# Optimization experiments

Measured on AMD Instinct MI355X. Metric: run time of the kernel, lower is better.

The kernel has to match this reference:

```python
import jax, jax.numpy as jnp
import numpy as np
from jax import lax

G, N, S, K, R = 8, 4096, 2048, 64, 0.4   # graphs, nodes/graph, fps samples (ratio=0.5), max neighbors, radius
EPER = 65536                              # edges per graph (avg degree 16)
C = 13                                    # num_classes


def setup_inputs():
    key = jax.random.key(0)
    ks = jax.random.split(key, 8)
    norm = jax.random.normal(ks[0], (G * N, 3), jnp.float32)
    pos = jax.random.uniform(ks[1], (G * N, 3), jnp.float32)
    x = jax.random.normal(ks[2], (G * N, 2), jnp.float32)
    e = jax.random.randint(ks[3], (2, G, EPER), 0, N)
    off = (jnp.arange(G) * N)[None, :, None]
    edge_index = (e + off).reshape(2, G * EPER).astype(jnp.int64)
    batch = jnp.repeat(jnp.arange(G), N).astype(jnp.int64)
    def lin(k, i, o):
        return jax.random.normal(k, (i, o), jnp.float32) / np.float32(np.sqrt(i))
    W1 = lin(ks[4], 8, 64);    b1 = jnp.zeros((64,), jnp.float32)
    W2 = lin(ks[5], 72, 128);  b2 = jnp.zeros((128,), jnp.float32)
    W3 = lin(ks[6], 139, 256); b3 = jnp.zeros((256,), jnp.float32)
    lin_w = lin(ks[7], 256, C); lin_b = jnp.zeros((C,), jnp.float32)
    return dict(norm=norm, pos=pos, x=x, edge_index=edge_index, batch=batch,
                W1=W1, b1=b1, W2=W2, b2=b2, W3=W3, b3=b3, lin_w=lin_w, lin_b=lin_b)


def _gcn(h, src, dst, ew, W, b, n):
    # GCNConv(normalize=False): out[dst] += ew * (h @ W)[src]; + bias
    m = (h @ W)[src] * ew[:, None]
    return jax.ops.segment_sum(m, dst, num_segments=n) + b


def _fps(p):  # farthest point sampling on one graph, p: [N,3] -> [S] local indices (start at node 0)
    def step(carry, _):
        mind, cur = carry
        d = jnp.sum((p - p[cur]) ** 2, axis=1)
        mind = jnp.minimum(mind, d)
        return (mind, jnp.argmax(mind).astype(jnp.int32)), cur
    _, idx = lax.scan(step, (jnp.full((N,), jnp.inf, p.dtype), jnp.int32(0)), None, length=S)
    return idx


def _radius(p, q):  # p [N,3], q [S,3] -> neighbor cols [S,K] (lowest-index-first within radius), valid mask
    d2 = jnp.sum((q[:, None, :] - p[None, :, :]) ** 2, axis=-1)  # [S,N]
    mask = d2 < R * R
    score = jnp.where(mask, N - jnp.arange(N, dtype=jnp.int32)[None, :], 0)
    vals, cols = lax.top_k(score, K)
    valid = vals > 0
    return jnp.where(valid, cols, 0), valid


def reference(norm, pos, x, edge_index, batch, W1, b1, W2, b2, W3, b3, lin_w, lin_b):
    NT = G * N
    inp = jnp.concatenate([norm, pos, x], axis=1)          # [NT, 8]
    src, dst = edge_index[0], edge_index[1]
    ew = jnp.ones((src.shape[0],), inp.dtype)
    # dropout is inactive at inference (training=False)
    h1 = jax.nn.relu(_gcn(inp, src, dst, ew, W1, b1, NT))  # [NT, 64]
    h1 = jnp.concatenate([h1, inp], axis=1)                # [NT, 72]
    h2 = jax.nn.relu(_gcn(h1, src, dst, ew, W2, b2, NT))   # [NT, 128]

    pg = pos.reshape(G, N, 3)
    pgs = lax.stop_gradient(pg)
    idx_loc = jax.vmap(_fps)(pgs)                          # [G, S] local indices
    q = jax.vmap(lambda p, i: p[i])(pg, idx_loc)           # [G, S, 3] sampled positions
    cols, valid = jax.vmap(_radius)(pgs, lax.stop_gradient(q))  # [G, S, K]

    # PointConv with identity local_nn/global_nn: max over neighbors of [x_j, pos_j - pos_i]
    hg = h2.reshape(G, N, 128)
    def pconv(h, p, qv, c, v):
        msg = jnp.concatenate([h[c], p[c] - qv[:, None, :]], axis=-1)  # [S, K, 131]
        msg = jnp.where(v[..., None], msg, -jnp.inf)
        return jnp.max(msg, axis=1)                                    # [S, 131]
    x_int = jax.vmap(pconv)(hg, pg, q, cols, valid).reshape(G * S, 131)

    # filter_adj: keep edges with both endpoints sampled, remap to new ids
    idx_flat = (idx_loc + (jnp.arange(G) * N)[:, None]).reshape(-1)    # [G*S] global indices
    mapping = jnp.full((NT,), -1, jnp.int32).at[idx_flat].set(jnp.arange(G * S, dtype=jnp.int32))
    ns, nd = mapping[src], mapping[dst]
    em = (ns >= 0) & (nd >= 0)
    ew3 = em.astype(inp.dtype)
    ns = jnp.where(em, ns, 0)
    nd = jnp.where(em, nd, 0)

    h3in = jnp.concatenate([x_int, inp[idx_flat]], axis=1)  # [G*S, 139]
    h3 = jax.nn.relu(_gcn(h3in, ns, nd, ew3, W3, b3, G * S))  # [G*S, 256]

    pooled = h3.reshape(G, S, 256).max(axis=1)              # global_max_pool -> [G, 256]
    logits = pooled @ lin_w + lin_b
    out = jax.nn.log_softmax(logits, axis=1)
    pred = jax.nn.softmax(out, axis=1)
    return (out, pred)
```

## Files before the change

### kernel.cpp

```cpp
#include <hip/hip_runtime.h>
#include <hip/hip_bf16.h>

constexpr int NG   = 8;
constexpr int NPG  = 4096;
constexpr int NT   = NG * NPG;
constexpr int NS   = 2048;
constexpr int GS   = NG * NS;
constexpr int KN   = 64;
constexpr int NE   = NG * 65536;
constexpr int NC   = 13;

__device__ __forceinline__ float inp_val(const float* norm, const float* pos, const float* x,
                                         int node, int dim) {
  if (dim < 3) return norm[(size_t)node * 3 + dim];
  if (dim < 6) return pos[(size_t)node * 3 + (dim - 3)];
  return x[(size_t)node * 2 + (dim - 6)];
}

__global__ void feat1_kernel(const float* __restrict__ norm, const float* __restrict__ pos,
                             const float* __restrict__ x, const float* __restrict__ W1,
                             float* __restrict__ t1) {
  int n = blockIdx.x, f = threadIdx.x;
  __shared__ float row[8];
  if (f < 8) row[f] = inp_val(norm, pos, x, n, f);
  __syncthreads();
  float acc = 0.f;
#pragma unroll
  for (int i = 0; i < 8; ++i) acc += row[i] * W1[i * 64 + f];
  t1[(size_t)n * 64 + f] = acc;
}

__global__ void feat2_kernel(const float* __restrict__ h1, const float* __restrict__ norm,
                             const float* __restrict__ pos, const float* __restrict__ x,
                             const float* __restrict__ W2, float* __restrict__ t2) {
  int n = blockIdx.x, f = threadIdx.x;
  __shared__ float row[72];
  if (f < 64) row[f] = h1[(size_t)n * 64 + f];
  else if (f < 72) row[f] = inp_val(norm, pos, x, n, f - 64);
  __syncthreads();
  float acc = 0.f;
#pragma unroll 8
  for (int i = 0; i < 72; ++i) acc += row[i] * W2[i * 128 + f];
  t2[(size_t)n * 128 + f] = acc;
}

__global__ void feat3_kernel(const float* __restrict__ xint, const int* __restrict__ idxf,
                             const float* __restrict__ norm, const float* __restrict__ pos,
                             const float* __restrict__ x, const float* __restrict__ W3,
                             float* __restrict__ t3) {
  int m = blockIdx.x, f = threadIdx.x;
  __shared__ float row[139];
  if (f < 131) row[f] = xint[(size_t)m * 131 + f];
  else if (f < 139) { int node = idxf[m]; row[f] = inp_val(norm, pos, x, node, f - 131); }
  __syncthreads();
  float acc = 0.f;
#pragma unroll 8
  for (int i = 0; i < 139; ++i) acc += row[i] * W3[i * 256 + f];
  t3[(size_t)m * 256 + f] = acc;
}

__global__ void deg1_kernel(const int* __restrict__ ei, int* __restrict__ deg) {
  int e = blockIdx.x * 256 + threadIdx.x;
  if (e < NE) atomicAdd(&deg[ei[NE + e]], 1);
}

__global__ void fill1_kernel(const int* __restrict__ ei, const int* __restrict__ off,
                             int* __restrict__ cur, int* __restrict__ el) {
  int e = blockIdx.x * 256 + threadIdx.x;
  if (e < NE) {
    int sN = ei[e], dN = ei[NE + e];
    int p = off[dN] + atomicAdd(&cur[dN], 1);
    el[p] = sN;
  }
}

__global__ void deg2_kernel(const int* __restrict__ ei, const int* __restrict__ mp,
                            int* __restrict__ deg) {
  int e = blockIdx.x * 256 + threadIdx.x;
  if (e < NE) {
    int ns = mp[ei[e]], nd = mp[ei[NE + e]];
    if (ns >= 0 && nd >= 0) atomicAdd(&deg[nd], 1);
  }
}

__global__ void fill2_kernel(const int* __restrict__ ei, const int* __restrict__ mp,
                             const int* __restrict__ off, int* __restrict__ cur,
                             int* __restrict__ el) {
  int e = blockIdx.x * 256 + threadIdx.x;
  if (e < NE) {
    int ns = mp[ei[e]], nd = mp[ei[NE + e]];
    if (ns >= 0 && nd >= 0) {
      int p = off[nd] + atomicAdd(&cur[nd], 1);
      el[p] = ns;
    }
  }
}

__global__ __launch_bounds__(1024) void scan_kernel(const int* __restrict__ in,
                                                    int* __restrict__ out, int n) {
  __shared__ int ls[1024];
  int tid = threadIdx.x;
  int per = (n + 1023) >> 10;
  int base = tid * per;
  int s = 0;
  for (int i = 0; i < per; ++i) { int idx = base + i; if (idx < n) s += in[idx]; }
  ls[tid] = s;
  __syncthreads();
  for (int d = 1; d < 1024; d <<= 1) {
    int v = (tid >= d) ? ls[tid - d] : 0;
    __syncthreads();
    ls[tid] += v;
    __syncthreads();
  }
  int excl = (tid == 0) ? 0 : ls[tid - 1];
  for (int i = 0; i < per; ++i) {
    int idx = base + i;
    if (idx < n) { out[idx] = excl; excl += in[idx]; }
  }
  if (tid == 1023) out[n] = ls[1023];
}

__global__ void agg_kernel(const float* __restrict__ t, const int* __restrict__ off,
                           const int* __restrict__ el, const float* __restrict__ b,
                           float* __restrict__ out, int F) {
  int node = blockIdx.x, f = threadIdx.x;
  int e0 = off[node], e1 = off[node + 1];
  float acc = 0.f;
  for (int j = e0; j < e1; ++j) acc += t[(size_t)el[j] * F + f];
  out[(size_t)node * F + f] = fmaxf(acc + b[f], 0.f);
}

__global__ __launch_bounds__(256, 1) void fps_kernel(const float* __restrict__ pos,
                                                     int* __restrict__ idxf,
                                                     float* __restrict__ qpos) {
  const int g = blockIdx.x;
  __shared__ float4 sq[2][4];
  __shared__ int sidx[2][4];
  __shared__ float4 qrec[NS];
  __shared__ int irec[NS];
  const float* pg = pos + (size_t)g * NPG * 3;
  const int tid = threadIdx.x;
  const int wave = tid >> 6, lane = tid & 63;
  const int p0 = tid * 16;

  float a[48];
  {
    const float4* pg4 = reinterpret_cast<const float4*>(pg + (size_t)p0 * 3);
#pragma unroll
    for (int j = 0; j < 12; ++j) {
      float4 t = pg4[j];
      a[4 * j + 0] = t.x; a[4 * j + 1] = t.y; a[4 * j + 2] = t.z; a[4 * j + 3] = t.w;
    }
  }
  float px[16], py[16], pz[16], mind[16];
#pragma unroll
  for (int i = 0; i < 16; ++i) {
    px[i] = a[3 * i]; py[i] = a[3 * i + 1]; pz[i] = a[3 * i + 2];
    mind[i] = __int_as_float(0x7f800000);
  }
  float cx = pg[0], cy = pg[1], cz = pg[2];
  int idx_sel = 0;

  for (int s = 0; s < NS; ++s) {
    if (tid == 0) { irec[s] = idx_sel; qrec[s] = make_float4(cx, cy, cz, 0.f); }
    float bestv = -1.f, bx = 0.f, by = 0.f, bz = 0.f;
    int bi = 0;
#pragma unroll
    for (int i = 0; i < 16; ++i) {
      float dx = __fsub_rn(px[i], cx);
      float dy = __fsub_rn(py[i], cy);
      float dz = __fsub_rn(pz[i], cz);
      float dd = __fadd_rn(__fadd_rn(__fmul_rn(dx, dx), __fmul_rn(dy, dy)), __fmul_rn(dz, dz));
      float nm = fminf(mind[i], dd);
      mind[i] = nm;
      bool gt = nm > bestv;
      bestv = gt ? nm : bestv;
      bx = gt ? px[i] : bx;
      by = gt ? py[i] : by;
      bz = gt ? pz[i] : bz;
      bi = gt ? i : bi;
    }
    float v = bestv;
    v = fmaxf(v, __int_as_float(__builtin_amdgcn_update_dpp(0, __float_as_int(v), 0x111, 0xF, 0xF, true)));
    v = fmaxf(v, __int_as_float(__builtin_amdgcn_update_dpp(0, __float_as_int(v), 0x112, 0xF, 0xF, true)));
    v = fmaxf(v, __int_as_float(__builtin_amdgcn_update_dpp(0, __float_as_int(v), 0x114, 0xF, 0xF, true)));
    v = fmaxf(v, __int_as_float(__builtin_amdgcn_update_dpp(0, __float_as_int(v), 0x118, 0xF, 0xF, true)));
    v = fmaxf(v, __int_as_float(__builtin_amdgcn_update_dpp(0, __float_as_int(v), 0x142, 0xF, 0xF, true)));
    v = fmaxf(v, __int_as_float(__builtin_amdgcn_update_dpp(0, __float_as_int(v), 0x143, 0xF, 0xF, true)));
    int maxbits = __builtin_amdgcn_readlane(__float_as_int(v), 63);
    float wavemax = __int_as_float(maxbits);
    unsigned long long ball = __ballot(bestv == wavemax);
    int winner = __ffsll(ball) - 1;
    int b = s & 1;
    if (lane == winner) {
      sq[b][wave] = make_float4(bx, by, bz, wavemax);
      sidx[b][wave] = p0 + bi;
    }
    __syncthreads();
    float4 q0 = sq[b][0], q1 = sq[b][1], q2 = sq[b][2], q3 = sq[b][3];
    float4 qs = q3;
    if (q2.w >= qs.w) qs = q2;
    if (q1.w >= qs.w) qs = q1;
    if (q0.w >= qs.w) qs = q0;
    cx = qs.x; cy = qs.y; cz = qs.z;
    if (tid == 0) {
      int i0 = sidx[b][0], i1 = sidx[b][1], i2 = sidx[b][2], i3 = sidx[b][3];
      float r = q3.w; int is = i3;
      if (q2.w >= r) { r = q2.w; is = i2; }
      if (q1.w >= r) { r = q1.w; is = i1; }
      if (q0.w >= r) { r = q0.w; is = i0; }
      idx_sel = is;
    }
  }
  __syncthreads();
  for (int j = tid; j < NS; j += 256) {
    idxf[g * NS + j] = g * NPG + irec[j];
    float4 q = qrec[j];
    size_t m = (size_t)(g * NS + j) * 3;
    qpos[m + 0] = q.x; qpos[m + 1] = q.y; qpos[m + 2] = q.z;
  }
}

__global__ __launch_bounds__(256) void radius_kernel(const float* __restrict__ pos,
                                                     const float* __restrict__ qpos,
                                                     int* __restrict__ cols,
                                                     int* __restrict__ cnt) {
  const int g = blockIdx.x;
  __shared__ float sx[NPG], sy[NPG], sz[NPG];
  const float* pg = pos + (size_t)g * NPG * 3;
  for (int i = threadIdx.x; i < NPG * 3; i += 256) {
    float v = pg[i]; int node = i / 3, c = i - node * 3;
    if (c == 0) sx[node] = v; else if (c == 1) sy[node] = v; else sz[node] = v;
  }
  __syncthreads();
  int m = g * NS + blockIdx.y * 256 + threadIdx.x;
  float qx = qpos[(size_t)m * 3], qy = qpos[(size_t)m * 3 + 1], qz = qpos[(size_t)m * 3 + 2];
  int* out = cols + (size_t)m * KN;
  int c = 0;
  for (int i = 0; i < NPG; ++i) {
    float dx = __fsub_rn(sx[i], qx);
    float dy = __fsub_rn(sy[i], qy);
    float dz = __fsub_rn(sz[i], qz);
    float d2 = __fadd_rn(__fadd_rn(__fmul_rn(dx, dx), __fmul_rn(dy, dy)), __fmul_rn(dz, dz));
    if (d2 < 0.16f) {
      out[c++] = i;
      if (c == KN) break;
    }
  }
  cnt[m] = c;
}

__global__ __launch_bounds__(64) void pointconv_kernel(const float* __restrict__ h2,
                                                       const float* __restrict__ pos,
                                                       const float* __restrict__ qpos,
                                                       const int* __restrict__ cols,
                                                       const int* __restrict__ cnt,
                                                       float* __restrict__ xint) {
  int m = blockIdx.x, t = threadIdx.x;
  int g = m / NS;
  int n = cnt[m];
  const int* cl = cols + (size_t)m * KN;
  float m0 = -INFINITY, m1 = -INFINITY, mp = -INFINITY;
  for (int k = 0; k < n; ++k) {
    int c = cl[k];
    size_t base = (size_t)(g * NPG + c);
    m0 = fmaxf(m0, h2[base * 128 + t]);
    m1 = fmaxf(m1, h2[base * 128 + 64 + t]);
    if (t < 3) mp = fmaxf(mp, pos[base * 3 + t]);
  }
  float* xo = xint + (size_t)m * 131;
  xo[t] = m0;
  xo[64 + t] = m1;
  if (t < 3) xo[128 + t] = __fsub_rn(mp, qpos[(size_t)m * 3 + t]);
}

__global__ void mapset_kernel(const int* __restrict__ idxf, int* __restrict__ mp) {
  int m = blockIdx.x * 256 + threadIdx.x;
  if (m < GS) mp[idxf[m]] = m;
}

__global__ void pool_kernel(const float* __restrict__ h3, float* __restrict__ pooled) {
  int g = blockIdx.x, ch = blockIdx.y, f = threadIdx.x;
  float mx = 0.f;
  size_t base = ((size_t)g * NS + (size_t)ch * 256) * 256 + f;
  for (int s = 0; s < 256; ++s) mx = fmaxf(mx, h3[base + (size_t)s * 256]);
  atomicMax((int*)pooled + g * 256 + f, __float_as_int(mx));
}

__global__ void head_kernel(const float* __restrict__ pooled, const float* __restrict__ lw,
                            const float* __restrict__ lb, float* __restrict__ outp) {
  __shared__ float lg[NG * NC];
  int t = threadIdx.x;
  if (t < NG * NC) {
    int g = t / NC, c = t % NC;
    float acc = lb[c];
    for (int k = 0; k < 256; ++k) acc += pooled[g * 256 + k] * lw[k * NC + c];
    lg[t] = acc;
  }
  __syncthreads();
  if (t < NG) {
    int g = t;
    float mx = -INFINITY;
    for (int c = 0; c < NC; ++c) mx = fmaxf(mx, lg[g * NC + c]);
    float sum = 0.f;
    for (int c = 0; c < NC; ++c) sum += expf(lg[g * NC + c] - mx);
    float lse = logf(sum);
    float ov[NC];
    float mx2 = -INFINITY;
    for (int c = 0; c < NC; ++c) {
      ov[c] = lg[g * NC + c] - mx - lse;
      outp[g * NC + c] = ov[c];
      mx2 = fmaxf(mx2, ov[c]);
    }
    float s2 = 0.f;
    for (int c = 0; c < NC; ++c) s2 += expf(ov[c] - mx2);
    for (int c = 0; c < NC; ++c) outp[NG * NC + g * NC + c] = expf(ov[c] - mx2) / s2;
  }
}

extern "C" void kernel_launch(void* const* d_in, const int* in_sizes, int n_in,
                              void* d_out, int out_size, void* d_ws, size_t ws_size,
                              hipStream_t stream) {
  const float* norm = (const float*)d_in[0];
  const float* pos  = (const float*)d_in[1];
  const float* x    = (const float*)d_in[2];
  const int* ei     = (const int*)d_in[3];
  const float* W1 = (const float*)d_in[5];
  const float* b1 = (const float*)d_in[6];
  const float* W2 = (const float*)d_in[7];
  const float* b2 = (const float*)d_in[8];
  const float* W3 = (const float*)d_in[9];
  const float* b3 = (const float*)d_in[10];
  const float* lw = (const float*)d_in[11];
  const float* lb = (const float*)d_in[12];
  float* outp = (float*)d_out;

  char* w = (char*)d_ws;
  size_t o = 0;
  auto alloc = [&](size_t bytes) -> void* {
    void* p = w + o;
    o = (o + bytes + 255) & ~(size_t)255;
    return p;
  };
  float* A    = (float*)alloc((size_t)NT * 128 * 4);
  float* Bf   = (float*)alloc((size_t)NT * 128 * 4);
  float* xint = (float*)alloc((size_t)GS * 131 * 4);
  int* cols   = (int*)alloc((size_t)GS * KN * 4);
  int* cnt    = (int*)alloc((size_t)GS * 4);
  int* deg1   = (int*)alloc((size_t)NT * 4);
  int* off1   = (int*)alloc((size_t)(NT + 1) * 4);
  int* cur1   = (int*)alloc((size_t)NT * 4);
  int* el1    = (int*)alloc((size_t)NE * 4);
  int* deg2   = (int*)alloc((size_t)GS * 4);
  int* off2   = (int*)alloc((size_t)(GS + 1) * 4);
  int* cur2   = (int*)alloc((size_t)GS * 4);
  int* el2    = (int*)alloc((size_t)NE * 4);
  int* idxf   = (int*)alloc((size_t)GS * 4);
  float* qpos = (float*)alloc((size_t)GS * 3 * 4);
  int* mapv   = (int*)alloc((size_t)NT * 4);
  float* pooled = (float*)alloc((size_t)NG * 256 * 4);

  hipMemsetAsync(deg1, 0, (size_t)NT * 4, stream);
  hipMemsetAsync(cur1, 0, (size_t)NT * 4, stream);
  hipMemsetAsync(deg2, 0, (size_t)GS * 4, stream);
  hipMemsetAsync(cur2, 0, (size_t)GS * 4, stream);
  hipMemsetAsync(mapv, 0xFF, (size_t)NT * 4, stream);
  hipMemsetAsync(pooled, 0, (size_t)NG * 256 * 4, stream);

  feat1_kernel<<<NT, 64, 0, stream>>>(norm, pos, x, W1, A);
  deg1_kernel<<<NE / 256, 256, 0, stream>>>(ei, deg1);
  scan_kernel<<<1, 1024, 0, stream>>>(deg1, off1, NT);
  fill1_kernel<<<NE / 256, 256, 0, stream>>>(ei, off1, cur1, el1);
  agg_kernel<<<NT, 64, 0, stream>>>(A, off1, el1, b1, Bf, 64);
  feat2_kernel<<<NT, 128, 0, stream>>>(Bf, norm, pos, x, W2, A);
  agg_kernel<<<NT, 128, 0, stream>>>(A, off1, el1, b2, Bf, 128);
  fps_kernel<<<NG, 256, 0, stream>>>(pos, idxf, qpos);
  radius_kernel<<<dim3(NG, NS / 256), 256, 0, stream>>>(pos, qpos, cols, cnt);
  pointconv_kernel<<<GS, 64, 0, stream>>>(Bf, pos, qpos, cols, cnt, xint);
  mapset_kernel<<<GS / 256, 256, 0, stream>>>(idxf, mapv);
  deg2_kernel<<<NE / 256, 256, 0, stream>>>(ei, mapv, deg2);
  scan_kernel<<<1, 1024, 0, stream>>>(deg2, off2, GS);
  fill2_kernel<<<NE / 256, 256, 0, stream>>>(ei, mapv, off2, cur2, el2);
  feat3_kernel<<<GS, 256, 0, stream>>>(xint, idxf, norm, pos, x, W3, A);
  agg_kernel<<<GS, 256, 0, stream>>>(A, off2, el2, b3, Bf, 256);
  pool_kernel<<<dim3(NG, NS / 256), 256, 0, stream>>>(Bf, pooled);
  head_kernel<<<1, 128, 0, stream>>>(pooled, lw, lb, outp);
}
```

Baseline: 2.437 ms.

## Widen FPS block to 512 threads and defer argmax coordinate tracking

The farthest point sampling kernel now runs 512 threads per graph, each owning 8 points instead of 16. This halves the serial per-thread distance work in each of the 2048 sequential steps. The per-point select chain for coordinates and index is replaced by a plain fmax in the inner loop. Only the winning lane recovers which point matched the wave max, using a bitmask and a select tree. The cost is an 8-way cross-wave reduction instead of 4-way, and a barrier spanning more waves each step.

```diff
diff --git a/kernel.cpp b/kernel.cpp
--- a/kernel.cpp
+++ b/kernel.cpp
@@ -130,31 +130,31 @@
   out[(size_t)node * F + f] = fmaxf(acc + b[f], 0.f);
 }
 
-__global__ __launch_bounds__(256, 1) void fps_kernel(const float* __restrict__ pos,
+__global__ __launch_bounds__(512, 1) void fps_kernel(const float* __restrict__ pos,
                                                      int* __restrict__ idxf,
                                                      float* __restrict__ qpos) {
   const int g = blockIdx.x;
-  __shared__ float4 sq[2][4];
-  __shared__ int sidx[2][4];
+  __shared__ float4 sq[2][8];
+  __shared__ int sidx[2][8];
   __shared__ float4 qrec[NS];
   __shared__ int irec[NS];
   const float* pg = pos + (size_t)g * NPG * 3;
   const int tid = threadIdx.x;
   const int wave = tid >> 6, lane = tid & 63;
-  const int p0 = tid * 16;
-
-  float a[48];
+  const int p0 = tid * 8;
+
+  float a[24];
   {
     const float4* pg4 = reinterpret_cast<const float4*>(pg + (size_t)p0 * 3);
 #pragma unroll
-    for (int j = 0; j < 12; ++j) {
+    for (int j = 0; j < 6; ++j) {
       float4 t = pg4[j];
       a[4 * j + 0] = t.x; a[4 * j + 1] = t.y; a[4 * j + 2] = t.z; a[4 * j + 3] = t.w;
     }
   }
-  float px[16], py[16], pz[16], mind[16];
+  float px[8], py[8], pz[8], mind[8];
 #pragma unroll
-  for (int i = 0; i < 16; ++i) {
+  for (int i = 0; i < 8; ++i) {
     px[i] = a[3 * i]; py[i] = a[3 * i + 1]; pz[i] = a[3 * i + 2];
     mind[i] = __int_as_float(0x7f800000);
   }
@@ -163,22 +163,16 @@
 
   for (int s = 0; s < NS; ++s) {
     if (tid == 0) { irec[s] = idx_sel; qrec[s] = make_float4(cx, cy, cz, 0.f); }
-    float bestv = -1.f, bx = 0.f, by = 0.f, bz = 0.f;
-    int bi = 0;
+    float bestv = -1.f;
 #pragma unroll
-    for (int i = 0; i < 16; ++i) {
+    for (int i = 0; i < 8; ++i) {
       float dx = __fsub_rn(px[i], cx);
       float dy = __fsub_rn(py[i], cy);
       float dz = __fsub_rn(pz[i], cz);
       float dd = __fadd_rn(__fadd_rn(__fmul_rn(dx, dx), __fmul_rn(dy, dy)), __fmul_rn(dz, dz));
       float nm = fminf(mind[i], dd);
       mind[i] = nm;
-      bool gt = nm > bestv;
-      bestv = gt ? nm : bestv;
-      bx = gt ? px[i] : bx;
-      by = gt ? py[i] : by;
-      bz = gt ? pz[i] : bz;
-      bi = gt ? i : bi;
+      bestv = fmaxf(bestv, nm);
     }
     float v = bestv;
     v = fmaxf(v, __int_as_float(__builtin_amdgcn_update_dpp(0, __float_as_int(v), 0x111, 0xF, 0xF, true)));
@@ -193,27 +187,52 @@
     int winner = __ffsll(ball) - 1;
     int b = s & 1;
     if (lane == winner) {
-      sq[b][wave] = make_float4(bx, by, bz, wavemax);
+      unsigned m8 = 0u;
+#pragma unroll
+      for (int i = 0; i < 8; ++i) m8 |= (mind[i] == wavemax ? 1u : 0u) << i;
+      int bi = __ffs(m8) - 1;
+      bool b0 = (bi & 1), b1 = (bi & 2), b2 = (bi & 4);
+      float x01 = b0 ? px[1] : px[0], x23 = b0 ? px[3] : px[2];
+      float x45 = b0 ? px[5] : px[4], x67 = b0 ? px[7] : px[6];
+      float y01 = b0 ? py[1] : py[0], y23 = b0 ? py[3] : py[2];
+      float y45 = b0 ? py[5] : py[4], y67 = b0 ? py[7] : py[6];
+      float z01 = b0 ? pz[1] : pz[0], z23 = b0 ? pz[3] : pz[2];
+      float z45 = b0 ? pz[5] : pz[4], z67 = b0 ? pz[7] : pz[6];
+      float x03 = b1 ? x23 : x01, x47 = b1 ? x67 : x45;
+      float y03 = b1 ? y23 : y01, y47 = b1 ? y67 : y45;
+      float z03 = b1 ? z23 : z01, z47 = b1 ? z67 : z45;
+      sq[b][wave] = make_float4(b2 ? x47 : x03, b2 ? y47 : y03, b2 ? z47 : z03, wavemax);
       sidx[b][wave] = p0 + bi;
     }
     __syncthreads();
-    float4 q0 = sq[b][0], q1 = sq[b][1], q2 = sq[b][2], q3 = sq[b][3];
-    float4 qs = q3;
-    if (q2.w >= qs.w) qs = q2;
-    if (q1.w >= qs.w) qs = q1;
-    if (q0.w >= qs.w) qs = q0;
+    float4 q0 = sq[b][0], q1 = sq[b][1];
+    float4 s01 = (q0.w >= q1.w) ? q0 : q1;
+    float4 q2 = sq[b][2], q3 = sq[b][3];
+    float4 s23 = (q2.w >= q3.w) ? q2 : q3;
+    float4 s03 = (s01.w >= s23.w) ? s01 : s23;
+    float4 q4 = sq[b][4], q5 = sq[b][5];
+    float4 s45 = (q4.w >= q5.w) ? q4 : q5;
+    float4 q6 = sq[b][6], q7 = sq[b][7];
+    float4 s67 = (q6.w >= q7.w) ? q6 : q7;
+    float4 s47 = (s45.w >= s67.w) ? s45 : s67;
+    float4 qs = (s03.w >= s47.w) ? s03 : s47;
     cx = qs.x; cy = qs.y; cz = qs.z;
     if (tid == 0) {
+      float k0 = sq[b][0].w, k1 = sq[b][1].w, k2 = sq[b][2].w, k3 = sq[b][3].w;
+      float k4 = sq[b][4].w, k5 = sq[b][5].w, k6 = sq[b][6].w, k7 = sq[b][7].w;
       int i0 = sidx[b][0], i1 = sidx[b][1], i2 = sidx[b][2], i3 = sidx[b][3];
-      float r = q3.w; int is = i3;
-      if (q2.w >= r) { r = q2.w; is = i2; }
-      if (q1.w >= r) { r = q1.w; is = i1; }
-      if (q0.w >= r) { r = q0.w; is = i0; }
-      idx_sel = is;
-    }
-  }
-  __syncthreads();
-  for (int j = tid; j < NS; j += 256) {
+      int i4 = sidx[b][4], i5 = sidx[b][5], i6 = sidx[b][6], i7 = sidx[b][7];
+      float ka = (k0 >= k1) ? k0 : k1;  int ia = (k0 >= k1) ? i0 : i1;
+      float kb = (k2 >= k3) ? k2 : k3;  int ib = (k2 >= k3) ? i2 : i3;
+      float kc = (ka >= kb) ? ka : kb;  int ic = (ka >= kb) ? ia : ib;
+      float kd = (k4 >= k5) ? k4 : k5;  int id = (k4 >= k5) ? i4 : i5;
+      float ke = (k6 >= k7) ? k6 : k7;  int ie = (k6 >= k7) ? i6 : i7;
+      float kf = (kd >= ke) ? kd : ke;  int if_ = (kd >= ke) ? id : ie;
+      idx_sel = (kc >= kf) ? ic : if_;
+    }
+  }
+  __syncthreads();
+  for (int j = tid; j < NS; j += 512) {
     idxf[g * NS + j] = g * NPG + irec[j];
     float4 q = qrec[j];
     size_t m = (size_t)(g * NS + j) * 3;
@@ -374,7 +393,7 @@
   agg_kernel<<<NT, 64, 0, stream>>>(A, off1, el1, b1, Bf, 64);
   feat2_kernel<<<NT, 128, 0, stream>>>(Bf, norm, pos, x, W2, A);
   agg_kernel<<<NT, 128, 0, stream>>>(A, off1, el1, b2, Bf, 128);
-  fps_kernel<<<NG, 256, 0, stream>>>(pos, idxf, qpos);
+  fps_kernel<<<NG, 512, 0, stream>>>(pos, idxf, qpos);
   radius_kernel<<<dim3(NG, NS / 256), 256, 0, stream>>>(pos, qpos, cols, cnt);
   pointconv_kernel<<<GS, 64, 0, stream>>>(Bf, pos, qpos, cols, cnt, xint);
   mapset_kernel<<<GS / 256, 256, 0, stream>>>(idxf, mapv);
```

Result: slower. 2.611 ms (+7.2%).

## Overlap serial FPS with feat1/degree counting and fold small kernels together

Applied to the files above, without the earlier changes.

The 8-block farthest-point-sampling kernel is merged into one launch with 504 extra blocks. Those extra blocks run the first feature transform and the first degree count in grid-stride loops, so this work fills otherwise idle compute units while FPS runs serially. The mapping scatter is moved into the radius kernel, and the second degree count is appended as extra blocks to the third feature transform, which removes two launches. In exchange, the worker blocks carry FPS's large shared-memory allocation, which limits their occupancy. The worker path also reads a shared row without a barrier, relying on a single wave running in lockstep.

```diff
diff --git a/kernel.cpp b/kernel.cpp
--- a/kernel.cpp
+++ b/kernel.cpp
@@ -9,6 +9,7 @@
 constexpr int KN   = 64;
 constexpr int NE   = NG * 65536;
 constexpr int NC   = 13;
+constexpr int NBW  = 504;
 
 __device__ __forceinline__ float inp_val(const float* norm, const float* pos, const float* x,
                                          int node, int dim) {
@@ -17,122 +18,28 @@
   return x[(size_t)node * 2 + (dim - 6)];
 }
 
-__global__ void feat1_kernel(const float* __restrict__ norm, const float* __restrict__ pos,
-                             const float* __restrict__ x, const float* __restrict__ W1,
-                             float* __restrict__ t1) {
-  int n = blockIdx.x, f = threadIdx.x;
-  __shared__ float row[8];
-  if (f < 8) row[f] = inp_val(norm, pos, x, n, f);
-  __syncthreads();
-  float acc = 0.f;
+__global__ __launch_bounds__(256, 1) void phaseA_kernel(
+    const float* __restrict__ pos, int* __restrict__ idxf, float* __restrict__ qpos,
+    const float* __restrict__ norm, const float* __restrict__ x,
+    const float* __restrict__ W1, float* __restrict__ t1,
+    const int* __restrict__ ei, int* __restrict__ deg) {
+  if (blockIdx.x >= 8) {
+    int wb = blockIdx.x - 8;
+    int sub = threadIdx.x >> 6;
+    int f = threadIdx.x & 63;
+    __shared__ float row[4][8];
+    for (int n0 = wb * 4; n0 < NT; n0 += NBW * 4) {
+      int n = n0 + sub;
+      if (f < 8) row[sub][f] = inp_val(norm, pos, x, n, f);
+      float acc = 0.f;
 #pragma unroll
-  for (int i = 0; i < 8; ++i) acc += row[i] * W1[i * 64 + f];
-  t1[(size_t)n * 64 + f] = acc;
-}
-
-__global__ void feat2_kernel(const float* __restrict__ h1, const float* __restrict__ norm,
-                             const float* __restrict__ pos, const float* __restrict__ x,
-                             const float* __restrict__ W2, float* __restrict__ t2) {
-  int n = blockIdx.x, f = threadIdx.x;
-  __shared__ float row[72];
-  if (f < 64) row[f] = h1[(size_t)n * 64 + f];
-  else if (f < 72) row[f] = inp_val(norm, pos, x, n, f - 64);
-  __syncthreads();
-  float acc = 0.f;
-#pragma unroll 8
-  for (int i = 0; i < 72; ++i) acc += row[i] * W2[i * 128 + f];
-  t2[(size_t)n * 128 + f] = acc;
-}
-
-__global__ void feat3_kernel(const float* __restrict__ xint, const int* __restrict__ idxf,
-                             const float* __restrict__ norm, const float* __restrict__ pos,
-                             const float* __restrict__ x, const float* __restrict__ W3,
-                             float* __restrict__ t3) {
-  int m = blockIdx.x, f = threadIdx.x;
-  __shared__ float row[139];
-  if (f < 131) row[f] = xint[(size_t)m * 131 + f];
-  else if (f < 139) { int node = idxf[m]; row[f] = inp_val(norm, pos, x, node, f - 131); }
-  __syncthreads();
-  float acc = 0.f;
-#pragma unroll 8
-  for (int i = 0; i < 139; ++i) acc += row[i] * W3[i * 256 + f];
-  t3[(size_t)m * 256 + f] = acc;
-}
-
-__global__ void deg1_kernel(const int* __restrict__ ei, int* __restrict__ deg) {
-  int e = blockIdx.x * 256 + threadIdx.x;
-  if (e < NE) atomicAdd(&deg[ei[NE + e]], 1);
-}
-
-__global__ void fill1_kernel(const int* __restrict__ ei, const int* __restrict__ off,
-                             int* __restrict__ cur, int* __restrict__ el) {
-  int e = blockIdx.x * 256 + threadIdx.x;
-  if (e < NE) {
-    int sN = ei[e], dN = ei[NE + e];
-    int p = off[dN] + atomicAdd(&cur[dN], 1);
-    el[p] = sN;
-  }
-}
-
-__global__ void deg2_kernel(const int* __restrict__ ei, const int* __restrict__ mp,
-                            int* __restrict__ deg) {
-  int e = blockIdx.x * 256 + threadIdx.x;
-  if (e < NE) {
-    int ns = mp[ei[e]], nd = mp[ei[NE + e]];
-    if (ns >= 0 && nd >= 0) atomicAdd(&deg[nd], 1);
-  }
-}
-
-__global__ void fill2_kernel(const int* __restrict__ ei, const int* __restrict__ mp,
-                             const int* __restrict__ off, int* __restrict__ cur,
-                             int* __restrict__ el) {
-  int e = blockIdx.x * 256 + threadIdx.x;
-  if (e < NE) {
-    int ns = mp[ei[e]], nd = mp[ei[NE + e]];
-    if (ns >= 0 && nd >= 0) {
-      int p = off[nd] + atomicAdd(&cur[nd], 1);
-      el[p] = ns;
-    }
-  }
-}
-
-__global__ __launch_bounds__(1024) void scan_kernel(const int* __restrict__ in,
-                                                    int* __restrict__ out, int n) {
-  __shared__ int ls[1024];
-  int tid = threadIdx.x;
-  int per = (n + 1023) >> 10;
-  int base = tid * per;
-  int s = 0;
-  for (int i = 0; i < per; ++i) { int idx = base + i; if (idx < n) s += in[idx]; }
-  ls[tid] = s;
-  __syncthreads();
-  for (int d = 1; d < 1024; d <<= 1) {
-    int v = (tid >= d) ? ls[tid - d] : 0;
-    __syncthreads();
-    ls[tid] += v;
-    __syncthreads();
-  }
-  int excl = (tid == 0) ? 0 : ls[tid - 1];
-  for (int i = 0; i < per; ++i) {
-    int idx = base + i;
-    if (idx < n) { out[idx] = excl; excl += in[idx]; }
-  }
-  if (tid == 1023) out[n] = ls[1023];
-}
-
-__global__ void agg_kernel(const float* __restrict__ t, const int* __restrict__ off,
-                           const int* __restrict__ el, const float* __restrict__ b,
-                           float* __restrict__ out, int F) {
-  int node = blockIdx.x, f = threadIdx.x;
-  int e0 = off[node], e1 = off[node + 1];
-  float acc = 0.f;
-  for (int j = e0; j < e1; ++j) acc += t[(size_t)el[j] * F + f];
-  out[(size_t)node * F + f] = fmaxf(acc + b[f], 0.f);
-}
-
-__global__ __launch_bounds__(256, 1) void fps_kernel(const float* __restrict__ pos,
-                                                     int* __restrict__ idxf,
-                                                     float* __restrict__ qpos) {
+      for (int i = 0; i < 8; ++i) acc += row[sub][i] * W1[i * 64 + f];
+      t1[(size_t)n * 64 + f] = acc;
+    }
+    for (int e = wb * 256 + threadIdx.x; e < NE; e += NBW * 256)
+      atomicAdd(&deg[ei[NE + e]], 1);
+    return;
+  }
   const int g = blockIdx.x;
   __shared__ float4 sq[2][4];
   __shared__ int sidx[2][4];
@@ -221,10 +128,106 @@
   }
 }
 
+__global__ void feat2_kernel(const float* __restrict__ h1, const float* __restrict__ norm,
+                             const float* __restrict__ pos, const float* __restrict__ x,
+                             const float* __restrict__ W2, float* __restrict__ t2) {
+  int n = blockIdx.x, f = threadIdx.x;
+  __shared__ float row[72];
+  if (f < 64) row[f] = h1[(size_t)n * 64 + f];
+  else if (f < 72) row[f] = inp_val(norm, pos, x, n, f - 64);
+  __syncthreads();
+  float acc = 0.f;
+#pragma unroll 8
+  for (int i = 0; i < 72; ++i) acc += row[i] * W2[i * 128 + f];
+  t2[(size_t)n * 128 + f] = acc;
+}
+
+__global__ void featdeg_kernel(const float* __restrict__ xint, const int* __restrict__ idxf,
+                               const float* __restrict__ norm, const float* __restrict__ pos,
+                               const float* __restrict__ x, const float* __restrict__ W3,
+                               float* __restrict__ t3,
+                               const int* __restrict__ ei, const int* __restrict__ mp,
+                               int* __restrict__ deg) {
+  if (blockIdx.x >= GS) {
+    int e = (blockIdx.x - GS) * 256 + threadIdx.x;
+    int ns = mp[ei[e]], nd = mp[ei[NE + e]];
+    if (ns >= 0 && nd >= 0) atomicAdd(&deg[nd], 1);
+    return;
+  }
+  int m = blockIdx.x, f = threadIdx.x;
+  __shared__ float row[139];
+  if (f < 131) row[f] = xint[(size_t)m * 131 + f];
+  else if (f < 139) { int node = idxf[m]; row[f] = inp_val(norm, pos, x, node, f - 131); }
+  __syncthreads();
+  float acc = 0.f;
+#pragma unroll 8
+  for (int i = 0; i < 139; ++i) acc += row[i] * W3[i * 256 + f];
+  t3[(size_t)m * 256 + f] = acc;
+}
+
+__global__ void fill1_kernel(const int* __restrict__ ei, const int* __restrict__ off,
+                             int* __restrict__ cur, int* __restrict__ el) {
+  int e = blockIdx.x * 256 + threadIdx.x;
+  if (e < NE) {
+    int sN = ei[e], dN = ei[NE + e];
+    int p = off[dN] + atomicAdd(&cur[dN], 1);
+    el[p] = sN;
+  }
+}
+
+__global__ void fill2_kernel(const int* __restrict__ ei, const int* __restrict__ mp,
+                             const int* __restrict__ off, int* __restrict__ cur,
+                             int* __restrict__ el) {
+  int e = blockIdx.x * 256 + threadIdx.x;
+  if (e < NE) {
+    int ns = mp[ei[e]], nd = mp[ei[NE + e]];
+    if (ns >= 0 && nd >= 0) {
+      int p = off[nd] + atomicAdd(&cur[nd], 1);
+      el[p] = ns;
+    }
+  }
+}
+
+__global__ __launch_bounds__(1024) void scan_kernel(const int* __restrict__ in,
+                                                    int* __restrict__ out, int n) {
+  __shared__ int ls[1024];
+  int tid = threadIdx.x;
+  int per = (n + 1023) >> 10;
+  int base = tid * per;
+  int s = 0;
+  for (int i = 0; i < per; ++i) { int idx = base + i; if (idx < n) s += in[idx]; }
+  ls[tid] = s;
+  __syncthreads();
+  for (int d = 1; d < 1024; d <<= 1) {
+    int v = (tid >= d) ? ls[tid - d] : 0;
+    __syncthreads();
+    ls[tid] += v;
+    __syncthreads();
+  }
+  int excl = (tid == 0) ? 0 : ls[tid - 1];
+  for (int i = 0; i < per; ++i) {
+    int idx = base + i;
+    if (idx < n) { out[idx] = excl; excl += in[idx]; }
+  }
+  if (tid == 1023) out[n] = ls[1023];
+}
+
+__global__ void agg_kernel(const float* __restrict__ t, const int* __restrict__ off,
+                           const int* __restrict__ el, const float* __restrict__ b,
+                           float* __restrict__ out, int F) {
+  int node = blockIdx.x, f = threadIdx.x;
+  int e0 = off[node], e1 = off[node + 1];
+  float acc = 0.f;
+  for (int j = e0; j < e1; ++j) acc += t[(size_t)el[j] * F + f];
+  out[(size_t)node * F + f] = fmaxf(acc + b[f], 0.f);
+}
+
 __global__ __launch_bounds__(256) void radius_kernel(const float* __restrict__ pos,
                                                      const float* __restrict__ qpos,
                                                      int* __restrict__ cols,
-                                                     int* __restrict__ cnt) {
+                                                     int* __restrict__ cnt,
+                                                     const int* __restrict__ idxf,
+                                                     int* __restrict__ mp) {
   const int g = blockIdx.x;
   __shared__ float sx[NPG], sy[NPG], sz[NPG];
   const float* pg = pos + (size_t)g * NPG * 3;
@@ -234,6 +237,7 @@
   }
   __syncthreads();
   int m = g * NS + blockIdx.y * 256 + threadIdx.x;
+  mp[idxf[m]] = m;
   float qx = qpos[(size_t)m * 3], qy = qpos[(size_t)m * 3 + 1], qz = qpos[(size_t)m * 3 + 2];
   int* out = cols + (size_t)m * KN;
   int c = 0;
@@ -272,11 +276,6 @@
   xo[t] = m0;
   xo[64 + t] = m1;
   if (t < 3) xo[128 + t] = __fsub_rn(mp, qpos[(size_t)m * 3 + t]);
-}
-
-__global__ void mapset_kernel(const int* __restrict__ idxf, int* __restrict__ mp) {
-  int m = blockIdx.x * 256 + threadIdx.x;
-  if (m < GS) mp[idxf[m]] = m;
 }
 
 __global__ void pool_kernel(const float* __restrict__ h3, float* __restrict__ pooled) {
@@ -367,21 +366,18 @@
   hipMemsetAsync(mapv, 0xFF, (size_t)NT * 4, stream);
   hipMemsetAsync(pooled, 0, (size_t)NG * 256 * 4, stream);
 
-  feat1_kernel<<<NT, 64, 0, stream>>>(norm, pos, x, W1, A);
-  deg1_kernel<<<NE / 256, 256, 0, stream>>>(ei, deg1);
+  phaseA_kernel<<<8 + NBW, 256, 0, stream>>>(pos, idxf, qpos, norm, x, W1, A, ei, deg1);
   scan_kernel<<<1, 1024, 0, stream>>>(deg1, off1, NT);
   fill1_kernel<<<NE / 256, 256, 0, stream>>>(ei, off1, cur1, el1);
   agg_kernel<<<NT, 64, 0, stream>>>(A, off1, el1, b1, Bf, 64);
   feat2_kernel<<<NT, 128, 0, stream>>>(Bf, norm, pos, x, W2, A);
   agg_kernel<<<NT, 128, 0, stream>>>(A, off1, el1, b2, Bf, 128);
-  fps_kernel<<<NG, 256, 0, stream>>>(pos, idxf, qpos);
-  radius_kernel<<<dim3(NG, NS / 256), 256, 0, stream>>>(pos, qpos, cols, cnt);
+  radius_kernel<<<dim3(NG, NS / 256), 256, 0, stream>>>(pos, qpos, cols, cnt, idxf, mapv);
   pointconv_kernel<<<GS, 64, 0, stream>>>(Bf, pos, qpos, cols, cnt, xint);
-  mapset_kernel<<<GS / 256, 256, 0, stream>>>(idxf, mapv);
-  deg2_kernel<<<NE / 256, 256, 0, stream>>>(ei, mapv, deg2);
+  featdeg_kernel<<<GS + NE / 256, 256, 0, stream>>>(xint, idxf, norm, pos, x, W3, A,
+                                                    ei, mapv, deg2);
   scan_kernel<<<1, 1024, 0, stream>>>(deg2, off2, GS);
   fill2_kernel<<<NE / 256, 256, 0, stream>>>(ei, mapv, off2, cur2, el2);
-  feat3_kernel<<<GS, 256, 0, stream>>>(xint, idxf, norm, pos, x, W3, A);
   agg_kernel<<<GS, 256, 0, stream>>>(A, off2, el2, b3, Bf, 256);
   pool_kernel<<<dim3(NG, NS / 256), 256, 0, stream>>>(Bf, pooled);
   head_kernel<<<1, 128, 0, stream>>>(pooled, lw, lb, outp);
```

Measured after the change: 2.357 ms. 3.3% less time.
